# Optimization experiments

Measured on AMD Instinct MI355X. Metric: run time of the kernel, lower is better.

Reference implementation:

```python
import jax, jax.numpy as jnp
import numpy as np

N_ATOMS = 100_000
N_BONDS = 200_000
MAX_NB = 6
HIDDEN = 300
ATOM_FD = 133
BOND_FD = 147
DEPTH = 3
ATOMS_PER_MOL = 20
N_MOLS = N_ATOMS // ATOMS_PER_MOL


def setup_inputs() -> dict:
    key = jax.random.key(0)
    ks = jax.random.split(key, 9)
    f_atoms = jax.random.normal(ks[0], (N_ATOMS, ATOM_FD), dtype=jnp.float32)
    f_bonds = jax.random.normal(ks[1], (N_BONDS, BOND_FD), dtype=jnp.float32)
    a2b = jax.random.randint(ks[2], (N_ATOMS, MAX_NB), 0, N_BONDS, dtype=jnp.int32)
    b2a = jax.random.randint(ks[3], (N_BONDS,), 0, N_ATOMS, dtype=jnp.int32)
    b2revb = jax.random.randint(ks[4], (N_BONDS,), 0, N_BONDS, dtype=jnp.int32)
    mol_ids = (jnp.arange(N_ATOMS, dtype=jnp.int32) // ATOMS_PER_MOL).astype(jnp.int32)
    W_i = jax.random.normal(ks[5], (BOND_FD, HIDDEN), dtype=jnp.float32) * 0.05
    W_h = jax.random.normal(ks[6], (HIDDEN, HIDDEN), dtype=jnp.float32) * 0.05
    W_o = jax.random.normal(ks[7], (ATOM_FD + HIDDEN, HIDDEN), dtype=jnp.float32) * 0.05
    b_o = jax.random.normal(ks[8], (HIDDEN,), dtype=jnp.float32) * 0.05
    return {"f_atoms": f_atoms, "f_bonds": f_bonds, "a2b": a2b, "b2a": b2a,
            "b2revb": b2revb, "mol_ids": mol_ids, "W_i": W_i, "W_h": W_h,
            "W_o": W_o, "b_o": b_o}


def reference(f_atoms, f_bonds, a2b, b2a, b2revb, mol_ids, W_i, W_h, W_o, b_o):
    # input = W_i(f_bonds); message = act(input)
    inp = f_bonds @ W_i                     # [n_bonds, H]
    message = jax.nn.relu(inp)
    for _ in range(DEPTH - 1):
        # padded-neighbor gather + sum over incoming bonds per atom
        a_message = message[a2b].sum(axis=1)          # [n_atoms, H]
        # forward gather minus reverse-bond message
        m = a_message[b2a] - message[b2revb]          # [n_bonds, H]
        message = jax.nn.relu(inp + m @ W_h)          # (dropout p=0 omitted)
    # final atom readout
    a_message = message[a2b].sum(axis=1)              # [n_atoms, H]
    a_input = jnp.concatenate([f_atoms, a_message], axis=1)  # [n_atoms, atom_fd+H]
    atom_hiddens = jax.nn.relu(a_input @ W_o + b_o)   # [n_atoms, H]
    # 'mean' pooling over each molecule's atoms (contiguous equal-size scopes)
    mol_sums = jax.ops.segment_sum(atom_hiddens, mol_ids, num_segments=N_MOLS)
    return mol_sums / ATOMS_PER_MOL                   # [n_mols, H]
```

## Files before the change

### kernel.cpp

```cpp
#include <hip/hip_runtime.h>
#include <hip/hip_bf16.h>
#include <hip/hip_fp8.h>

#define N_ATOMS 100000
#define N_BONDS 200000
#define MAX_NB 6
#define HIDDEN 300
#define HP 320
#define CH 40
#define ATOM_FD 133
#define BOND_FD 147
#define N_MOLS 5000
#define APM 20

#define NT32 10
#define KKI32 10
#define KKH32 20
#define KKO32 28

using bf16 = __hip_bfloat16;
typedef __attribute__((ext_vector_type(8))) short short8v;
typedef __attribute__((ext_vector_type(4))) float float4v;
typedef __attribute__((ext_vector_type(2))) float float2v;
typedef __attribute__((ext_vector_type(16))) float float16v;
typedef unsigned int u32;
typedef unsigned short u16;
typedef unsigned char u8;

__device__ __forceinline__ float us2f(u16 u) {
    union { u32 i; float f; } v; v.i = ((u32)u) << 16; return v.f;
}
__device__ __forceinline__ u16 f2us(float f) {
    bf16 h = __float2bfloat16(f);
    return *(u16*)&h;
}
__device__ __forceinline__ u32 pack2(float a, float b) {
    return (u32)f2us(a) | ((u32)f2us(b) << 16);
}
__device__ __forceinline__ uint2 pack4(const float4v& a) {
    uint2 o; o.x = pack2(a[0], a[1]); o.y = pack2(a[2], a[3]); return o;
}

#if defined(__has_builtin)
#if __has_builtin(__builtin_amdgcn_cvt_f32_fp8) && __has_builtin(__builtin_amdgcn_cvt_pk_fp8_f32)
#define HW_FP8 1
#endif
#if __has_builtin(__builtin_amdgcn_cvt_pk_f32_fp8)
#define HW_FP8_PK 1
#endif
#endif

__device__ __forceinline__ void f8x4_to_f32(u32 p, float* o) {
#if defined(HW_FP8_PK)
    float2v lo = __builtin_amdgcn_cvt_pk_f32_fp8(p, false);
    float2v hi = __builtin_amdgcn_cvt_pk_f32_fp8(p, true);
    o[0] = lo[0]; o[1] = lo[1]; o[2] = hi[0]; o[3] = hi[1];
#elif defined(HW_FP8)
    o[0] = __builtin_amdgcn_cvt_f32_fp8(p, 0);
    o[1] = __builtin_amdgcn_cvt_f32_fp8(p, 1);
    o[2] = __builtin_amdgcn_cvt_f32_fp8(p, 2);
    o[3] = __builtin_amdgcn_cvt_f32_fp8(p, 3);
#else
#pragma unroll
    for (int i = 0; i < 4; ++i) {
        __hip_fp8_e4m3 h; h.__x = (u8)(p >> (8 * i));
        o[i] = (float)h;
    }
#endif
}
__device__ __forceinline__ u32 f32x4_to_f8(float a, float b, float c, float d) {
#ifdef HW_FP8
    u32 r = __builtin_amdgcn_cvt_pk_fp8_f32(a, b, 0u, false);
    r = __builtin_amdgcn_cvt_pk_fp8_f32(c, d, r, true);
    return r;
#else
    __hip_fp8_e4m3 ha(a), hb(b), hc(c), hd(d);
    return (u32)ha.__x | ((u32)hb.__x << 8) | ((u32)hc.__x << 16) | ((u32)hd.__x << 24);
#endif
}
__device__ __forceinline__ void f8x16_to_f32(uint4 u, float* o) {
    f8x4_to_f32(u.x, o); f8x4_to_f32(u.y, o + 4);
    f8x4_to_f32(u.z, o + 8); f8x4_to_f32(u.w, o + 12);
}
__device__ __forceinline__ u32 relu_f8x4(u32 u) {
    u32 m = (u >> 7) & 0x01010101u;
    return u & ~(m * 255u);
}
__device__ __forceinline__ uint4 relu_f8x16(uint4 u) {
    u.x = relu_f8x4(u.x); u.y = relu_f8x4(u.y);
    u.z = relu_f8x4(u.z); u.w = relu_f8x4(u.w);
    return u;
}

__global__ __launch_bounds__(64) void pack_w32(const float* __restrict__ src,
                                               short* __restrict__ dst,
                                               int Ksrc, int mode) {
    int kk = blockIdx.x / NT32, nt = blockIdx.x % NT32;
    int lane = threadIdx.x;
    int col = nt * 32 + (lane & 31);
#pragma unroll
    for (int j = 0; j < 8; ++j) {
        int k = kk * 16 + (lane >> 5) * 8 + j;
        float v = 0.f;
        if (k < Ksrc && col < HIDDEN) {
            int krow = k;
            if (mode == 2) krow = (k < HIDDEN) ? (ATOM_FD + k) : (k - HIDDEN);
            v = src[krow * HIDDEN + col];
        }
        dst[(((kk * NT32 + nt) << 6) + lane) * 8 + j] = (short)f2us(v);
    }
}

__global__ __launch_bounds__(256) void k0_zero(float* __restrict__ out) {
    int i = blockIdx.x * 256 + threadIdx.x;
    if (i < N_MOLS * HIDDEN) out[i] = 0.f;
}

__global__ __launch_bounds__(320) void k1_input(const float* __restrict__ fb,
                                                const short8v* __restrict__ WiP,
                                                u8* __restrict__ inp8) {
    __shared__ __align__(16) char sm[32 * 640];
    const int tid = threadIdx.x;
    const long base = (long)blockIdx.x * 32;
    const float4* src4 = (const float4*)(fb + base * BOND_FD);
#pragma unroll
    for (int it = 0; it < 4; ++it) {
        int idx = tid + it * 320;
        if (idx < 1176) {
            float4 v = src4[idx];
            int f = idx * 4;
#pragma unroll
            for (int e = 0; e < 4; ++e) {
                int g = f + e;
                int r = g / BOND_FD, c = g - r * BOND_FD;
                int byte = r * 320 + c * 2;
                *(u16*)(sm + (byte ^ ((r & 7) << 4))) = f2us(((const float*)&v)[e]);
            }
        }
    }
    for (int i = tid; i < 32 * 13; i += 320) {
        int r = i / 13, c = BOND_FD + i % 13;
        int byte = r * 320 + c * 2;
        *(u16*)(sm + (byte ^ ((r & 7) << 4))) = 0;
    }
    __syncthreads();

    const int lane = tid & 63, wave = tid >> 6;
    const int row = lane & 31, hi = lane >> 5;
    const int nt0 = wave * 2;
    float16v acc0, acc1;
#pragma unroll
    for (int q = 0; q < 16; ++q) { acc0[q] = 0.f; acc1[q] = 0.f; }
    for (int kk = 0; kk < KKI32; ++kk) {
        int byte = row * 320 + kk * 32 + hi * 16;
        short8v a = *(const short8v*)(sm + (byte ^ ((row & 7) << 4)));
        short8v w0 = WiP[((kk * NT32 + nt0) << 6) + lane];
        short8v w1 = WiP[((kk * NT32 + nt0 + 1) << 6) + lane];
        acc0 = __builtin_amdgcn_mfma_f32_32x32x16_bf16(w0, a, acc0, 0, 0, 0);
        acc1 = __builtin_amdgcn_mfma_f32_32x32x16_bf16(w1, a, acc1, 0, 0, 0);
    }
    __syncthreads();
#pragma unroll
    for (int t = 0; t < 2; ++t) {
#pragma unroll
        for (int q = 0; q < 4; ++q) {
            int colb = (nt0 + t) * 32 + q * 8 + hi * 4;
            float a0 = (t == 0 ? acc0[4 * q + 0] : acc1[4 * q + 0]);
            float a1 = (t == 0 ? acc0[4 * q + 1] : acc1[4 * q + 1]);
            float a2 = (t == 0 ? acc0[4 * q + 2] : acc1[4 * q + 2]);
            float a3 = (t == 0 ? acc0[4 * q + 3] : acc1[4 * q + 3]);
            *(u32*)(sm + row * 336 + colb) = f32x4_to_f8(a0, a1, a2, a3);
        }
    }
    __syncthreads();
#pragma unroll
    for (int it = 0; it < 2; ++it) {
        int i = tid + it * 320;
        int r = i / 20, c = i % 20;
        uint4 v = *(const uint4*)(sm + r * 336 + c * 16);
        ((uint4*)(inp8 + (base + r) * 320))[c] = v;
    }
}

template<int RELU>
__global__ __launch_bounds__(256, 8) void k2_gather(const u8* __restrict__ src,
                                                    const int* __restrict__ a2b,
                                                    u8* __restrict__ dst) {
    int id = blockIdx.x * 256 + threadIdx.x;
    int atom = id / 10, c2 = id % 10;
    if (atom >= N_ATOMS) return;
    const int* nb = a2b + atom * MAX_NB;
    float s[32];
#pragma unroll
    for (int q = 0; q < 32; ++q) s[q] = 0.f;
#pragma unroll
    for (int j = 0; j < MAX_NB; ++j) {
        const uint4* rp = (const uint4*)(src + (long)nb[j] * 320);
        uint4 u0 = rp[2 * c2];
        uint4 u1 = rp[2 * c2 + 1];
        if (RELU) { u0 = relu_f8x16(u0); u1 = relu_f8x16(u1); }
        float v[16];
        f8x16_to_f32(u0, v);
#pragma unroll
        for (int q = 0; q < 16; ++q) s[q] += v[q];
        f8x16_to_f32(u1, v);
#pragma unroll
        for (int q = 0; q < 16; ++q) s[16 + q] += v[q];
    }
    uint4 o0, o1;
    o0.x = f32x4_to_f8(s[0], s[1], s[2], s[3]);
    o0.y = f32x4_to_f8(s[4], s[5], s[6], s[7]);
    o0.z = f32x4_to_f8(s[8], s[9], s[10], s[11]);
    o0.w = f32x4_to_f8(s[12], s[13], s[14], s[15]);
    o1.x = f32x4_to_f8(s[16], s[17], s[18], s[19]);
    o1.y = f32x4_to_f8(s[20], s[21], s[22], s[23]);
    o1.z = f32x4_to_f8(s[24], s[25], s[26], s[27]);
    o1.w = f32x4_to_f8(s[28], s[29], s[30], s[31]);
    uint4* dp = (uint4*)(dst + (long)atom * 320);
    dp[2 * c2] = o0;
    dp[2 * c2 + 1] = o1;
}

template<int RELUSRC>
__global__ __launch_bounds__(320) void kzf_update(const u8* __restrict__ inp8,
                                                  const u8* __restrict__ AM,
                                                  const u8* __restrict__ msgsrc,
                                                  const int* __restrict__ b2a,
                                                  const int* __restrict__ b2revb,
                                                  const short8v* __restrict__ WhP,
                                                  u8* __restrict__ msgdst) {
    __shared__ __align__(16) char sm[32 * 640];
    const int tid = threadIdx.x;
    const long base = (long)blockIdx.x * 32;

#pragma unroll
    for (int it = 0; it < 2; ++it) {
        int i = tid + it * 320;
        int r = i / 20, c = i % 20;
        long b = base + r;
        int ia = b2a[b], ir = b2revb[b];
        uint4 ua = ((const uint4*)(AM + (long)ia * 320))[c];
        uint4 um = ((const uint4*)(msgsrc + (long)ir * 320))[c];
        if (RELUSRC) um = relu_f8x16(um);
        float av[16], mv[16];
        f8x16_to_f32(ua, av);
        f8x16_to_f32(um, mv);
        uint4 o0, o1;
        o0.x = pack2(av[0] - mv[0], av[1] - mv[1]);
        o0.y = pack2(av[2] - mv[2], av[3] - mv[3]);
        o0.z = pack2(av[4] - mv[4], av[5] - mv[5]);
        o0.w = pack2(av[6] - mv[6], av[7] - mv[7]);
        o1.x = pack2(av[8] - mv[8], av[9] - mv[9]);
        o1.y = pack2(av[10] - mv[10], av[11] - mv[11]);
        o1.z = pack2(av[12] - mv[12], av[13] - mv[13]);
        o1.w = pack2(av[14] - mv[14], av[15] - mv[15]);
        int byte = r * 640 + c * 32;
        int swz = (r & 7) << 4;
        *(uint4*)(sm + (byte ^ swz)) = o0;
        *(uint4*)(sm + ((byte + 16) ^ swz)) = o1;
    }
    __syncthreads();

    const int lane = tid & 63, wave = tid >> 6;
    const int row = lane & 31, hi = lane >> 5;
    const int nt0 = wave * 2;
    float16v acc0, acc1;
#pragma unroll
    for (int q = 0; q < 16; ++q) { acc0[q] = 0.f; acc1[q] = 0.f; }
    for (int kk = 0; kk < KKH32; ++kk) {
        int byte = row * 640 + kk * 32 + hi * 16;
        short8v a = *(const short8v*)(sm + (byte ^ ((row & 7) << 4)));
        short8v w0 = WhP[((kk * NT32 + nt0) << 6) + lane];
        short8v w1 = WhP[((kk * NT32 + nt0 + 1) << 6) + lane];
        acc0 = __builtin_amdgcn_mfma_f32_32x32x16_bf16(w0, a, acc0, 0, 0, 0);
        acc1 = __builtin_amdgcn_mfma_f32_32x32x16_bf16(w1, a, acc1, 0, 0, 0);
    }
    __syncthreads();
#pragma unroll
    for (int t = 0; t < 2; ++t) {
#pragma unroll
        for (int q = 0; q < 4; ++q) {
            int colb = (nt0 + t) * 32 + q * 8 + hi * 4;
            u32 u = *(const u32*)(inp8 + (base + row) * 320 + colb);
            float iv[4];
            f8x4_to_f32(u, iv);
            float a0 = (t == 0 ? acc0[4 * q + 0] : acc1[4 * q + 0]);
            float a1 = (t == 0 ? acc0[4 * q + 1] : acc1[4 * q + 1]);
            float a2 = (t == 0 ? acc0[4 * q + 2] : acc1[4 * q + 2]);
            float a3 = (t == 0 ? acc0[4 * q + 3] : acc1[4 * q + 3]);
            float v0 = fmaxf(a0 + iv[0], 0.f);
            float v1 = fmaxf(a1 + iv[1], 0.f);
            float v2 = fmaxf(a2 + iv[2], 0.f);
            float v3 = fmaxf(a3 + iv[3], 0.f);
            *(u32*)(sm + row * 336 + colb) = f32x4_to_f8(v0, v1, v2, v3);
        }
    }
    __syncthreads();
#pragma unroll
    for (int it = 0; it < 2; ++it) {
        int i = tid + it * 320;
        int r = i / 20, c = i % 20;
        uint4 v = *(const uint4*)(sm + r * 336 + c * 16);
        ((uint4*)(msgdst + (base + r) * 320))[c] = v;
    }
}

__global__ __launch_bounds__(320) void k4_gemm(const float* __restrict__ fa,
                                               const u8* __restrict__ msg,
                                               const int* __restrict__ a2b,
                                               const short8v* __restrict__ WoP,
                                               const float* __restrict__ bo,
                                               float* __restrict__ out) {
    __shared__ __align__(16) char sm[32 * 896];
    const int tid = threadIdx.x;
    const long base = (long)blockIdx.x * 32;
#pragma unroll
    for (int it = 0; it < 2; ++it) {
        int i = tid + it * 320;
        if (i < 608) {
            int row = i / 19, c = i % 19;
            long atom = base + row;
            const int* nb = a2b + atom * MAX_NB;
            int n0 = nb[0], n1 = nb[1], n2 = nb[2];
            int n3 = nb[3], n4 = nb[4], n5 = nb[5];
            uint4 u0 = ((const uint4*)(msg + (long)n0 * 320))[c];
            uint4 u1 = ((const uint4*)(msg + (long)n1 * 320))[c];
            uint4 u2 = ((const uint4*)(msg + (long)n2 * 320))[c];
            uint4 u3 = ((const uint4*)(msg + (long)n3 * 320))[c];
            uint4 u4 = ((const uint4*)(msg + (long)n4 * 320))[c];
            uint4 u5 = ((const uint4*)(msg + (long)n5 * 320))[c];
            float s[16], v[16];
            f8x16_to_f32(u0, s);
            f8x16_to_f32(u1, v);
#pragma unroll
            for (int q = 0; q < 16; ++q) s[q] += v[q];
            f8x16_to_f32(u2, v);
#pragma unroll
            for (int q = 0; q < 16; ++q) s[q] += v[q];
            f8x16_to_f32(u3, v);
#pragma unroll
            for (int q = 0; q < 16; ++q) s[q] += v[q];
            f8x16_to_f32(u4, v);
#pragma unroll
            for (int q = 0; q < 16; ++q) s[q] += v[q];
            f8x16_to_f32(u5, v);
#pragma unroll
            for (int q = 0; q < 16; ++q) s[q] += v[q];
            uint4 o0, o1;
            o0.x = pack2(s[0], s[1]);  o0.y = pack2(s[2], s[3]);
            o0.z = pack2(s[4], s[5]);  o0.w = pack2(s[6], s[7]);
            o1.x = pack2(s[8], s[9]);  o1.y = pack2(s[10], s[11]);
            o1.z = pack2(s[12], s[13]); o1.w = pack2(s[14], s[15]);
            int byte = row * 896 + c * 32;
            int swz = (row & 7) << 4;
            *(uint4*)(sm + (byte ^ swz)) = o0;
            if (c < 18) {
                *(uint4*)(sm + ((byte + 16) ^ swz)) = o1;
            } else {
                *(uint2*)(sm + ((byte + 16) ^ swz)) = make_uint2(o1.x, o1.y);
            }
        }
    }
    const float4* src4 = (const float4*)(fa + base * ATOM_FD);
#pragma unroll
    for (int it = 0; it < 4; ++it) {
        int idx = tid + it * 320;
        if (idx < 1064) {
            float4 v = src4[idx];
            int f = idx * 4;
#pragma unroll
            for (int e = 0; e < 4; ++e) {
                int g = f + e;
                int r = g / ATOM_FD, c2 = g - r * ATOM_FD;
                int byte = r * 896 + (HIDDEN + c2) * 2;
                *(u16*)(sm + (byte ^ ((r & 7) << 4))) = f2us(((const float*)&v)[e]);
            }
        }
    }
    for (int i = tid; i < 480; i += 320) {
        int r = i / 15, c2 = ATOM_FD + i % 15;
        int byte = r * 896 + (HIDDEN + c2) * 2;
        *(u16*)(sm + (byte ^ ((r & 7) << 4))) = 0;
    }
    __syncthreads();

    const int lane = tid & 63, wave = tid >> 6;
    const int row = lane & 31, hi = lane >> 5;
    const int nt0 = wave * 2;
    float16v acc0, acc1;
#pragma unroll
    for (int q = 0; q < 16; ++q) { acc0[q] = 0.f; acc1[q] = 0.f; }
    for (int kk = 0; kk < KKO32; ++kk) {
        int byte = row * 896 + kk * 32 + hi * 16;
        short8v a = *(const short8v*)(sm + (byte ^ ((row & 7) << 4)));
        short8v w0 = WoP[((kk * NT32 + nt0) << 6) + lane];
        short8v w1 = WoP[((kk * NT32 + nt0 + 1) << 6) + lane];
        acc0 = __builtin_amdgcn_mfma_f32_32x32x16_bf16(w0, a, acc0, 0, 0, 0);
        acc1 = __builtin_amdgcn_mfma_f32_32x32x16_bf16(w1, a, acc1, 0, 0, 0);
    }
    __syncthreads();
#pragma unroll
    for (int t = 0; t < 2; ++t) {
#pragma unroll
        for (int q = 0; q < 4; ++q) {
            int colb = (nt0 + t) * 32 + q * 8 + hi * 4;
            float4v v;
#pragma unroll
            for (int d = 0; d < 4; ++d) {
                float bias = (colb + d < HIDDEN) ? bo[colb + d] : 0.f;
                float av = (t == 0 ? acc0[4 * q + d] : acc1[4 * q + d]);
                v[d] = fmaxf(av + bias, 0.f);
            }
            int byte = row * 640 + colb * 2;
            *(uint2*)(sm + (byte ^ ((row & 7) << 4))) = pack4(v);
        }
    }
    __syncthreads();
    const int mfirst = (int)(base / APM);
    const int mlast = (int)((base + 31) / APM);
    const int nseg = mlast - mfirst + 1;
    for (int idx = tid; idx < nseg * HIDDEN; idx += 320) {
        int s = idx / HIDDEN, col = idx % HIDDEN;
        int m = mfirst + s;
        long a0 = (long)m * APM; if (a0 < base) a0 = base;
        long a1 = (long)(m + 1) * APM; if (a1 > base + 32) a1 = base + 32;
        float sum = 0.f;
        for (long a = a0; a < a1; ++a) {
            int r = (int)(a - base);
            int byte = r * 640 + col * 2;
            sum += us2f(*(const u16*)(sm + (byte ^ ((r & 7) << 4))));
        }
        atomicAdd(out + (long)m * HIDDEN + col, sum * (1.f / APM));
    }
}

extern "C" void kernel_launch(void* const* d_in, const int* in_sizes, int n_in,
                              void* d_out, int out_size, void* d_ws, size_t ws_size,
                              hipStream_t stream) {
    const float* f_atoms = (const float*)d_in[0];
    const float* f_bonds = (const float*)d_in[1];
    const int* a2b = (const int*)d_in[2];
    const int* b2a = (const int*)d_in[3];
    const int* b2revb = (const int*)d_in[4];
    const float* Wi = (const float*)d_in[6];
    const float* Wh = (const float*)d_in[7];
    const float* Wo = (const float*)d_in[8];
    const float* bo = (const float*)d_in[9];
    float* out = (float*)d_out;

    char* ws = (char*)d_ws;
    size_t off = 0;
    auto alloc = [&](size_t bytes) {
        void* p = ws + off;
        off = (off + bytes + 255) & ~(size_t)255;
        return p;
    };
    u8* inp8  = (u8*)alloc((size_t)N_BONDS * 320);
    u8* msgA  = (u8*)alloc((size_t)N_BONDS * 320);
    u8* msgB  = (u8*)alloc((size_t)N_BONDS * 320);
    u8* AM    = (u8*)alloc((size_t)N_ATOMS * 320);
    short* WiP32 = (short*)alloc((size_t)KKI32 * NT32 * 64 * 8 * sizeof(short));
    short* WhP32 = (short*)alloc((size_t)KKH32 * NT32 * 64 * 8 * sizeof(short));
    short* WoP32 = (short*)alloc((size_t)KKO32 * NT32 * 64 * 8 * sizeof(short));

    pack_w32<<<KKI32 * NT32, 64, 0, stream>>>(Wi, WiP32, BOND_FD, 0);
    pack_w32<<<KKH32 * NT32, 64, 0, stream>>>(Wh, WhP32, HIDDEN, 0);
    pack_w32<<<KKO32 * NT32, 64, 0, stream>>>(Wo, WoP32, ATOM_FD + HIDDEN, 2);
    k0_zero<<<(N_MOLS * HIDDEN + 255) / 256, 256, 0, stream>>>(out);

    k1_input<<<N_BONDS / 32, 320, 0, stream>>>(f_bonds, (const short8v*)WiP32, inp8);

    const int g2 = (N_ATOMS * 10 + 255) / 256;
    k2_gather<1><<<g2, 256, 0, stream>>>(inp8, a2b, AM);
    kzf_update<1><<<N_BONDS / 32, 320, 0, stream>>>(inp8, AM, inp8, b2a, b2revb,
                                                    (const short8v*)WhP32, msgA);
    k2_gather<0><<<g2, 256, 0, stream>>>(msgA, a2b, AM);
    kzf_update<0><<<N_BONDS / 32, 320, 0, stream>>>(inp8, AM, msgA, b2a, b2revb,
                                                    (const short8v*)WhP32, msgB);
    k4_gemm<<<N_ATOMS / 32, 320, 0, stream>>>(f_atoms, msgB, a2b,
                                              (const short8v*)WoP32, bo, out);
}
```

Measured before the change: 441.5 us.

## Process two bond tiles per block, prefetching second tile's gathers during first MFMA

The bond update kernel now handles two 32-bond tiles per block. It issues the gathered loads for the second tile before running the MFMA loop on the first tile, and converts the second tile while the first tile's epilogue runs. The aim is to hide gather latency behind matrix math. In exchange it doubles shared memory per block to 40KB and raises register pressure, which may lower occupancy, and it halves the grid.

```diff
diff --git a/kernel.cpp b/kernel.cpp
--- a/kernel.cpp
+++ b/kernel.cpp
@@ -229,80 +229,120 @@
                                                   const int* __restrict__ b2revb,
                                                   const short8v* __restrict__ WhP,
                                                   u8* __restrict__ msgdst) {
-    __shared__ __align__(16) char sm[32 * 640];
+    __shared__ __align__(16) char smA[32 * 640];
+    __shared__ __align__(16) char smB[32 * 640];
     const int tid = threadIdx.x;
-    const long base = (long)blockIdx.x * 32;
-
-#pragma unroll
-    for (int it = 0; it < 2; ++it) {
-        int i = tid + it * 320;
-        int r = i / 20, c = i % 20;
-        long b = base + r;
-        int ia = b2a[b], ir = b2revb[b];
-        uint4 ua = ((const uint4*)(AM + (long)ia * 320))[c];
-        uint4 um = ((const uint4*)(msgsrc + (long)ir * 320))[c];
-        if (RELUSRC) um = relu_f8x16(um);
-        float av[16], mv[16];
-        f8x16_to_f32(ua, av);
-        f8x16_to_f32(um, mv);
-        uint4 o0, o1;
-        o0.x = pack2(av[0] - mv[0], av[1] - mv[1]);
-        o0.y = pack2(av[2] - mv[2], av[3] - mv[3]);
-        o0.z = pack2(av[4] - mv[4], av[5] - mv[5]);
-        o0.w = pack2(av[6] - mv[6], av[7] - mv[7]);
-        o1.x = pack2(av[8] - mv[8], av[9] - mv[9]);
-        o1.y = pack2(av[10] - mv[10], av[11] - mv[11]);
-        o1.z = pack2(av[12] - mv[12], av[13] - mv[13]);
-        o1.w = pack2(av[14] - mv[14], av[15] - mv[15]);
-        int byte = r * 640 + c * 32;
-        int swz = (r & 7) << 4;
-        *(uint4*)(sm + (byte ^ swz)) = o0;
-        *(uint4*)(sm + ((byte + 16) ^ swz)) = o1;
-    }
-    __syncthreads();
-
+    const long base0 = (long)blockIdx.x * 64;
+    const long base1 = base0 + 32;
     const int lane = tid & 63, wave = tid >> 6;
     const int row = lane & 31, hi = lane >> 5;
     const int nt0 = wave * 2;
+
+    auto stage_load = [&](long tb, uint4* ua, uint4* um) {
+#pragma unroll
+        for (int it = 0; it < 2; ++it) {
+            int i = tid + it * 320;
+            int r = i / 20, c = i % 20;
+            long b = tb + r;
+            ua[it] = ((const uint4*)(AM + (long)b2a[b] * 320))[c];
+            um[it] = ((const uint4*)(msgsrc + (long)b2revb[b] * 320))[c];
+        }
+    };
+    auto convert = [&](char* sm, const uint4* ua, const uint4* um) {
+#pragma unroll
+        for (int it = 0; it < 2; ++it) {
+            int i = tid + it * 320;
+            int r = i / 20, c = i % 20;
+            uint4 a = ua[it], m = um[it];
+            if (RELUSRC) m = relu_f8x16(m);
+            float av[16], mv[16];
+            f8x16_to_f32(a, av);
+            f8x16_to_f32(m, mv);
+            uint4 o0, o1;
+            o0.x = pack2(av[0] - mv[0], av[1] - mv[1]);
+            o0.y = pack2(av[2] - mv[2], av[3] - mv[3]);
+            o0.z = pack2(av[4] - mv[4], av[5] - mv[5]);
+            o0.w = pack2(av[6] - mv[6], av[7] - mv[7]);
+            o1.x = pack2(av[8] - mv[8], av[9] - mv[9]);
+            o1.y = pack2(av[10] - mv[10], av[11] - mv[11]);
+            o1.z = pack2(av[12] - mv[12], av[13] - mv[13]);
+            o1.w = pack2(av[14] - mv[14], av[15] - mv[15]);
+            int byte = r * 640 + c * 32;
+            int swz = (r & 7) << 4;
+            *(uint4*)(sm + (byte ^ swz)) = o0;
+            *(uint4*)(sm + ((byte + 16) ^ swz)) = o1;
+        }
+    };
+    auto mfma_tile = [&](const char* sm, float16v& a0, float16v& a1) {
+        for (int kk = 0; kk < KKH32; ++kk) {
+            int byte = row * 640 + kk * 32 + hi * 16;
+            short8v a = *(const short8v*)(sm + (byte ^ ((row & 7) << 4)));
+            short8v w0 = WhP[((kk * NT32 + nt0) << 6) + lane];
+            short8v w1 = WhP[((kk * NT32 + nt0 + 1) << 6) + lane];
+            a0 = __builtin_amdgcn_mfma_f32_32x32x16_bf16(w0, a, a0, 0, 0, 0);
+            a1 = __builtin_amdgcn_mfma_f32_32x32x16_bf16(w1, a, a1, 0, 0, 0);
+        }
+    };
+    auto epilogue = [&](char* sm, long tb, const float16v& a0, const float16v& a1) {
+#pragma unroll
+        for (int t = 0; t < 2; ++t) {
+#pragma unroll
+            for (int q = 0; q < 4; ++q) {
+                int colb = (nt0 + t) * 32 + q * 8 + hi * 4;
+                u32 u = *(const u32*)(inp8 + (tb + row) * 320 + colb);
+                float iv[4];
+                f8x4_to_f32(u, iv);
+                float x0 = (t == 0 ? a0[4 * q + 0] : a1[4 * q + 0]);
+                float x1 = (t == 0 ? a0[4 * q + 1] : a1[4 * q + 1]);
+                float x2 = (t == 0 ? a0[4 * q + 2] : a1[4 * q + 2]);
+                float x3 = (t == 0 ? a0[4 * q + 3] : a1[4 * q + 3]);
+                float v0 = fmaxf(x0 + iv[0], 0.f);
+                float v1 = fmaxf(x1 + iv[1], 0.f);
+                float v2 = fmaxf(x2 + iv[2], 0.f);
+                float v3 = fmaxf(x3 + iv[3], 0.f);
+                *(u32*)(sm + row * 336 + colb) = f32x4_to_f8(v0, v1, v2, v3);
+            }
+        }
+    };
+    auto store_tile = [&](const char* sm, long tb) {
+#pragma unroll
+        for (int it = 0; it < 2; ++it) {
+            int i = tid + it * 320;
+            int r = i / 20, c = i % 20;
+            uint4 v = *(const uint4*)(sm + r * 336 + c * 16);
+            ((uint4*)(msgdst + (tb + r) * 320))[c] = v;
+        }
+    };
+
+    uint4 ua0[2], um0[2];
+    stage_load(base0, ua0, um0);
+    convert(smA, ua0, um0);
+    __syncthreads();
+
+    uint4 ua1[2], um1[2];
+    stage_load(base1, ua1, um1);
+    __builtin_amdgcn_sched_barrier(0);
+
     float16v acc0, acc1;
 #pragma unroll
     for (int q = 0; q < 16; ++q) { acc0[q] = 0.f; acc1[q] = 0.f; }
-    for (int kk = 0; kk < KKH32; ++kk) {
-        int byte = row * 640 + kk * 32 + hi * 16;
-        short8v a = *(const short8v*)(sm + (byte ^ ((row & 7) << 4)));
-        short8v w0 = WhP[((kk * NT32 + nt0) << 6) + lane];
-        short8v w1 = WhP[((kk * NT32 + nt0 + 1) << 6) + lane];
-        acc0 = __builtin_amdgcn_mfma_f32_32x32x16_bf16(w0, a, acc0, 0, 0, 0);
-        acc1 = __builtin_amdgcn_mfma_f32_32x32x16_bf16(w1, a, acc1, 0, 0, 0);
-    }
-    __syncthreads();
-#pragma unroll
-    for (int t = 0; t < 2; ++t) {
-#pragma unroll
-        for (int q = 0; q < 4; ++q) {
-            int colb = (nt0 + t) * 32 + q * 8 + hi * 4;
-            u32 u = *(const u32*)(inp8 + (base + row) * 320 + colb);
-            float iv[4];
-            f8x4_to_f32(u, iv);
-            float a0 = (t == 0 ? acc0[4 * q + 0] : acc1[4 * q + 0]);
-            float a1 = (t == 0 ? acc0[4 * q + 1] : acc1[4 * q + 1]);
-            float a2 = (t == 0 ? acc0[4 * q + 2] : acc1[4 * q + 2]);
-            float a3 = (t == 0 ? acc0[4 * q + 3] : acc1[4 * q + 3]);
-            float v0 = fmaxf(a0 + iv[0], 0.f);
-            float v1 = fmaxf(a1 + iv[1], 0.f);
-            float v2 = fmaxf(a2 + iv[2], 0.f);
-            float v3 = fmaxf(a3 + iv[3], 0.f);
-            *(u32*)(sm + row * 336 + colb) = f32x4_to_f8(v0, v1, v2, v3);
-        }
-    }
-    __syncthreads();
-#pragma unroll
-    for (int it = 0; it < 2; ++it) {
-        int i = tid + it * 320;
-        int r = i / 20, c = i % 20;
-        uint4 v = *(const uint4*)(sm + r * 336 + c * 16);
-        ((uint4*)(msgdst + (base + r) * 320))[c] = v;
-    }
+    mfma_tile(smA, acc0, acc1);
+    __syncthreads();
+
+    epilogue(smA, base0, acc0, acc1);
+    convert(smB, ua1, um1);
+    __syncthreads();
+
+    store_tile(smA, base0);
+    float16v bcc0, bcc1;
+#pragma unroll
+    for (int q = 0; q < 16; ++q) { bcc0[q] = 0.f; bcc1[q] = 0.f; }
+    mfma_tile(smB, bcc0, bcc1);
+    __syncthreads();
+
+    epilogue(smB, base1, bcc0, bcc1);
+    __syncthreads();
+    store_tile(smB, base1);
 }
 
 __global__ __launch_bounds__(320) void k4_gemm(const float* __restrict__ fa,
@@ -472,10 +512,10 @@
 
     const int g2 = (N_ATOMS * 10 + 255) / 256;
     k2_gather<1><<<g2, 256, 0, stream>>>(inp8, a2b, AM);
-    kzf_update<1><<<N_BONDS / 32, 320, 0, stream>>>(inp8, AM, inp8, b2a, b2revb,
+    kzf_update<1><<<N_BONDS / 64, 320, 0, stream>>>(inp8, AM, inp8, b2a, b2revb,
                                                     (const short8v*)WhP32, msgA);
     k2_gather<0><<<g2, 256, 0, stream>>>(msgA, a2b, AM);
-    kzf_update<0><<<N_BONDS / 32, 320, 0, stream>>>(inp8, AM, msgA, b2a, b2revb,
+    kzf_update<0><<<N_BONDS / 64, 320, 0, stream>>>(inp8, AM, msgA, b2a, b2revb,
                                                     (const short8v*)WhP32, msgB);
     k4_gemm<<<N_ATOMS / 32, 320, 0, stream>>>(f_atoms, msgB, a2b,
                                               (const short8v*)WoP32, bo, out);
```

Measured after the change: 518.3 us. 17.4% more time.
